# Kernel tuning notes

Measured on AMD Instinct MI355X. Metric: run time of the kernel, lower is better.

Reference implementation:

```python
import jax, jax.numpy as jnp
import numpy as np

B, C, D = 1024, 50000, 256
LR = 0.5


def setup_inputs() -> dict:
    key = jax.random.key(0)
    kx, kl, kc = jax.random.split(key, 3)
    x = jax.random.normal(kx, (B, D), dtype=jnp.float32)
    labels = jax.random.randint(kl, (B,), 0, C)
    y = jax.nn.one_hot(labels, C, dtype=jnp.float32)  # [B, C] one-hot
    center = jax.random.normal(kc, (C, D), dtype=jnp.float32) * 0.05
    return {"x": x, "y": y, "center": center}


def reference(x, y, center):
    # dists = x - y @ center : gather each sample's class center via one-hot GEMM
    dists = x - jnp.matmul(y, center)                      # [B, D]
    # center gradient: scatter-add of -dists into class rows via one-hot GEMM
    grads = jnp.matmul(-y.T, dists)                        # [C, D]
    new_center = center - LR * grads                       # manual SGD update (assign_sub)
    loss = jnp.linalg.norm(dists, axis=1, keepdims=True)   # [B, 1]
    num_sams = jnp.sum(y, axis=0, keepdims=True) + 1.0     # [1, C]
    loss = loss / num_sams                                 # broadcasts to [B, C] as in original
    return loss, new_center
```

## Files before the change

kernel.cpp:

```cpp
#include <hip/hip_runtime.h>
#include <math.h>

#define BB 1024
#define CC 50000
#define DD 256
#define LRATE 0.5f

__global__ void k_zero_counts(int* __restrict__ counts) {
    int i = blockIdx.x * blockDim.x + threadIdx.x;
    if (i < CC) counts[i] = 0;
}

__global__ void k_labels(const float* __restrict__ y,
                         int* __restrict__ labels,
                         int* __restrict__ counts) {
    int b = blockIdx.x;
    const float4* row = (const float4*)(y + (size_t)b * CC);
    int found = -1;
    for (int i = threadIdx.x; i < CC / 4; i += blockDim.x) {
        float4 v = row[i];
        if (v.x > 0.5f) found = 4 * i;
        else if (v.y > 0.5f) found = 4 * i + 1;
        else if (v.z > 0.5f) found = 4 * i + 2;
        else if (v.w > 0.5f) found = 4 * i + 3;
    }
    __shared__ int s_lab;
    if (threadIdx.x == 0) s_lab = 0;
    __syncthreads();
    if (found >= 0) s_lab = found;
    __syncthreads();
    if (threadIdx.x == 0) {
        labels[b] = s_lab;
        atomicAdd(&counts[s_lab], 1);
    }
}

__global__ void k_inv(const int* __restrict__ counts, float* __restrict__ inv_ns) {
    int i = blockIdx.x * blockDim.x + threadIdx.x;
    if (i < CC) inv_ns[i] = 1.0f / ((float)counts[i] + 1.0f);
}

__global__ void k_copy_center(const float4* __restrict__ src, float4* __restrict__ dst) {
    const int n4 = CC * DD / 4;
    int i = blockIdx.x * blockDim.x + threadIdx.x;
    if (i < n4) dst[i] = src[i];
}

__global__ void k_update(const float* __restrict__ x,
                         const float* __restrict__ center,
                         const int* __restrict__ labels,
                         float* __restrict__ out_center,
                         float* __restrict__ loss_norm) {
    int b = blockIdx.x;
    int d = threadIdx.x;
    int lab = labels[b];
    float dist = x[(size_t)b * DD + d] - center[(size_t)lab * DD + d];
    atomicAdd(&out_center[(size_t)lab * DD + d], LRATE * dist);

    float sq = dist * dist;
    #pragma unroll
    for (int off = 32; off > 0; off >>= 1)
        sq += __shfl_down(sq, off, 64);
    __shared__ float s[4];
    int wave = threadIdx.x >> 6;
    if ((threadIdx.x & 63) == 0) s[wave] = sq;
    __syncthreads();
    if (threadIdx.x == 0)
        loss_norm[b] = sqrtf(s[0] + s[1] + s[2] + s[3]);
}

#define ROWS_PER_BLK 16
__global__ void k_loss(const float* __restrict__ loss_norm,
                       const float* __restrict__ inv_ns,
                       float* __restrict__ out_loss) {
    const int C4 = CC / 4;
    int c4 = blockIdx.x * blockDim.x + threadIdx.x;
    if (c4 >= C4) return;
    float4 inv = ((const float4*)inv_ns)[c4];
    int b0 = blockIdx.y * ROWS_PER_BLK;
    #pragma unroll
    for (int r = 0; r < ROWS_PER_BLK; ++r) {
        int b = b0 + r;
        float ln = loss_norm[b];
        float4 o;
        o.x = ln * inv.x; o.y = ln * inv.y; o.z = ln * inv.z; o.w = ln * inv.w;
        ((float4*)(out_loss + (size_t)b * CC))[c4] = o;
    }
}

extern "C" void kernel_launch(void* const* d_in, const int* in_sizes, int n_in,
                              void* d_out, int out_size, void* d_ws, size_t ws_size,
                              hipStream_t stream) {
    const float* x      = (const float*)d_in[0];
    const float* y      = (const float*)d_in[1];
    const float* center = (const float*)d_in[2];

    float* out_loss   = (float*)d_out;
    float* out_center = (float*)d_out + (size_t)BB * CC;

    char* ws = (char*)d_ws;
    int*   counts    = (int*)ws;
    float* inv_ns    = (float*)(ws + ((size_t)CC * 4 + 255) / 256 * 256);
    char*  ws2       = (char*)inv_ns + ((size_t)CC * 4 + 255) / 256 * 256;
    int*   labels    = (int*)ws2;
    float* loss_norm = (float*)(ws2 + 4096);

    k_zero_counts<<<(CC + 255) / 256, 256, 0, stream>>>(counts);
    k_labels<<<BB, 256, 0, stream>>>(y, labels, counts);
    k_inv<<<(CC + 255) / 256, 256, 0, stream>>>(counts, inv_ns);
    k_copy_center<<<(CC * DD / 4 + 255) / 256, 256, 0, stream>>>(
        (const float4*)center, (float4*)out_center);
    k_update<<<BB, DD, 0, stream>>>(x, center, labels, out_center, loss_norm);

    dim3 lgrid((CC / 4 + 255) / 256, BB / ROWS_PER_BLK);
    k_loss<<<lgrid, 256, 0, stream>>>(loss_norm, inv_ns, out_loss);
}
```

Before: 447.6 us.

## Fuse kernels and early-exit one-hot label scan on first nonzero chunk

Merges the counts zeroing into the center copy kernel, fuses label finding with the center update, and folds the inverse-count computation into the loss kernel, cutting six launches to three. The label scan now reads y as integer bits and stops after the chunk that holds the nonzero entry, so on average only part of each one-hot row is read instead of the full 200KB row. The early exit relies on y being exactly one-hot with a single nonzero per row; rows with no nonzero still scan fully and fall back to label 0.

After: 420.0 us. 6.2% less time.

```diff
diff --git a/kernel.cpp b/kernel.cpp
--- a/kernel.cpp
+++ b/kernel.cpp
@@ -6,54 +6,53 @@
 #define DD 256
 #define LRATE 0.5f
 
-__global__ void k_zero_counts(int* __restrict__ counts) {
+__global__ void k_init(const float4* __restrict__ center,
+                       float4* __restrict__ out_center,
+                       int4* __restrict__ counts) {
     int i = blockIdx.x * blockDim.x + threadIdx.x;
-    if (i < CC) counts[i] = 0;
+    const int n4 = CC * DD / 4;
+    if (i < n4) out_center[i] = center[i];
+    if (i < CC / 4)
+        counts[i] = make_int4(0, 0, 0, 0);
 }
 
-__global__ void k_labels(const float* __restrict__ y,
-                         int* __restrict__ labels,
-                         int* __restrict__ counts) {
+#define CHUNK_ITERS 8
+__global__ void k_labels_update(const unsigned int* __restrict__ y,
+                                const float* __restrict__ x,
+                                const float* __restrict__ center,
+                                float* __restrict__ out_center,
+                                int* __restrict__ counts,
+                                float* __restrict__ loss_norm) {
     int b = blockIdx.x;
-    const float4* row = (const float4*)(y + (size_t)b * CC);
-    int found = -1;
-    for (int i = threadIdx.x; i < CC / 4; i += blockDim.x) {
-        float4 v = row[i];
-        if (v.x > 0.5f) found = 4 * i;
-        else if (v.y > 0.5f) found = 4 * i + 1;
-        else if (v.z > 0.5f) found = 4 * i + 2;
-        else if (v.w > 0.5f) found = 4 * i + 3;
+    const uint4* row = (const uint4*)(y + (size_t)b * CC);
+    __shared__ int s_lab;
+    __shared__ float s_part[4];
+    if (threadIdx.x == 0) s_lab = -1;
+    __syncthreads();
+
+    const int C4 = CC / 4;
+    for (int base = 0; base < C4; base += 256 * CHUNK_ITERS) {
+        #pragma unroll
+        for (int j = 0; j < CHUNK_ITERS; ++j) {
+            int i = base + j * 256 + threadIdx.x;
+            if (i < C4) {
+                uint4 v = row[i];
+                if (v.x | v.y | v.z | v.w) {
+                    s_lab = 4 * i + (v.x ? 0 : (v.y ? 1 : (v.z ? 2 : 3)));
+                }
+            }
+        }
+        __syncthreads();
+        int found = s_lab;
+        __syncthreads();
+        if (found >= 0) break;
     }
-    __shared__ int s_lab;
-    if (threadIdx.x == 0) s_lab = 0;
-    __syncthreads();
-    if (found >= 0) s_lab = found;
-    __syncthreads();
-    if (threadIdx.x == 0) {
-        labels[b] = s_lab;
-        atomicAdd(&counts[s_lab], 1);
-    }
-}
 
-__global__ void k_inv(const int* __restrict__ counts, float* __restrict__ inv_ns) {
-    int i = blockIdx.x * blockDim.x + threadIdx.x;
-    if (i < CC) inv_ns[i] = 1.0f / ((float)counts[i] + 1.0f);
-}
+    int lab = s_lab;
+    if (lab < 0) lab = 0;
+    if (threadIdx.x == 0) atomicAdd(&counts[lab], 1);
 
-__global__ void k_copy_center(const float4* __restrict__ src, float4* __restrict__ dst) {
-    const int n4 = CC * DD / 4;
-    int i = blockIdx.x * blockDim.x + threadIdx.x;
-    if (i < n4) dst[i] = src[i];
-}
-
-__global__ void k_update(const float* __restrict__ x,
-                         const float* __restrict__ center,
-                         const int* __restrict__ labels,
-                         float* __restrict__ out_center,
-                         float* __restrict__ loss_norm) {
-    int b = blockIdx.x;
     int d = threadIdx.x;
-    int lab = labels[b];
     float dist = x[(size_t)b * DD + d] - center[(size_t)lab * DD + d];
     atomicAdd(&out_center[(size_t)lab * DD + d], LRATE * dist);
 
@@ -61,22 +60,25 @@
     #pragma unroll
     for (int off = 32; off > 0; off >>= 1)
         sq += __shfl_down(sq, off, 64);
-    __shared__ float s[4];
-    int wave = threadIdx.x >> 6;
-    if ((threadIdx.x & 63) == 0) s[wave] = sq;
+    if ((threadIdx.x & 63) == 0) s_part[threadIdx.x >> 6] = sq;
     __syncthreads();
     if (threadIdx.x == 0)
-        loss_norm[b] = sqrtf(s[0] + s[1] + s[2] + s[3]);
+        loss_norm[b] = sqrtf(s_part[0] + s_part[1] + s_part[2] + s_part[3]);
 }
 
 #define ROWS_PER_BLK 16
 __global__ void k_loss(const float* __restrict__ loss_norm,
-                       const float* __restrict__ inv_ns,
+                       const int* __restrict__ counts,
                        float* __restrict__ out_loss) {
     const int C4 = CC / 4;
     int c4 = blockIdx.x * blockDim.x + threadIdx.x;
     if (c4 >= C4) return;
-    float4 inv = ((const float4*)inv_ns)[c4];
+    int4 cnt = ((const int4*)counts)[c4];
+    float4 inv;
+    inv.x = 1.0f / ((float)cnt.x + 1.0f);
+    inv.y = 1.0f / ((float)cnt.y + 1.0f);
+    inv.z = 1.0f / ((float)cnt.z + 1.0f);
+    inv.w = 1.0f / ((float)cnt.w + 1.0f);
     int b0 = blockIdx.y * ROWS_PER_BLK;
     #pragma unroll
     for (int r = 0; r < ROWS_PER_BLK; ++r) {
@@ -92,26 +94,21 @@
                               void* d_out, int out_size, void* d_ws, size_t ws_size,
                               hipStream_t stream) {
     const float* x      = (const float*)d_in[0];
-    const float* y      = (const float*)d_in[1];
+    const unsigned int* y = (const unsigned int*)d_in[1];
     const float* center = (const float*)d_in[2];
 
     float* out_loss   = (float*)d_out;
     float* out_center = (float*)d_out + (size_t)BB * CC;
 
-    char* ws = (char*)d_ws;
-    int*   counts    = (int*)ws;
-    float* inv_ns    = (float*)(ws + ((size_t)CC * 4 + 255) / 256 * 256);
-    char*  ws2       = (char*)inv_ns + ((size_t)CC * 4 + 255) / 256 * 256;
-    int*   labels    = (int*)ws2;
-    float* loss_norm = (float*)(ws2 + 4096);
+    int*   counts    = (int*)d_ws;
+    float* loss_norm = (float*)((char*)d_ws + 256 * 1024);
 
-    k_zero_counts<<<(CC + 255) / 256, 256, 0, stream>>>(counts);
-    k_labels<<<BB, 256, 0, stream>>>(y, labels, counts);
-    k_inv<<<(CC + 255) / 256, 256, 0, stream>>>(counts, inv_ns);
-    k_copy_center<<<(CC * DD / 4 + 255) / 256, 256, 0, stream>>>(
-        (const float4*)center, (float4*)out_center);
-    k_update<<<BB, DD, 0, stream>>>(x, center, labels, out_center, loss_norm);
+    k_init<<<CC * DD / 4 / 256, 256, 0, stream>>>(
+        (const float4*)center, (float4*)out_center, (int4*)counts);
+
+    k_labels_update<<<BB, DD, 0, stream>>>(
+        y, x, center, out_center, counts, loss_norm);
 
     dim3 lgrid((CC / 4 + 255) / 256, BB / ROWS_PER_BLK);
-    k_loss<<<lgrid, 256, 0, stream>>>(loss_norm, inv_ns, out_loss);
+    k_loss<<<lgrid, 256, 0, stream>>>(loss_norm, counts, out_loss);
 }
```
